# Kernel tuning notes

Measured on AMD Instinct MI355X. Metric: run time of the kernel, lower is better.

Reference implementation:

```python
import jax, jax.numpy as jnp
import numpy as np

B, N, H, HID, LOCALITY = 2, 4096, 4, 256, 30.0
VD = HID // H
F32_MAX = jnp.finfo(jnp.float32).max


def setup_inputs() -> dict:
    key = jax.random.key(0)
    k1, k2, k3, k4 = jax.random.split(key, 4)
    m_dist = jax.random.uniform(k1, (B, N, N), dtype=jnp.float32)  # pairwise distances (b,N,N)
    x = jax.random.normal(k2, (B, N, HID), dtype=jnp.float32)
    r = jax.random.normal(k3, (1, H, 1, 1), dtype=jnp.float32)  # learned per-head distance scale
    # lecun_normal: std = 1/sqrt(fan_in), fan_in = HID
    weight = jax.random.normal(k4, (H, HID, VD), dtype=jnp.float32) / np.sqrt(HID)
    return {"m_dist": m_dist, "x": x, "r": r, "weight": weight}


def reference(m_dist, x, r, weight):
    # scaled distance per head: (b,h,n,n)
    scaled = m_dist[:, None, :, :] * (r ** 2)
    # percentile-thresholded local mask (linear interpolation, per row)
    thresh = jnp.percentile(scaled, LOCALITY, axis=-1, keepdims=True, method="linear")
    scaled = jnp.where(scaled <= thresh, scaled, F32_MAX)
    att = jax.nn.softmax(-scaled, axis=-1)  # (b,h,n,n)
    value = jnp.einsum("bnj,hjk->bhnk", x, weight)  # (b,h,n,v)
    out = jnp.einsum("bhnj,bhjd->bhnd", att, value)  # (b,h,n,v)
    out = jnp.transpose(out, (0, 2, 1, 3)).reshape(out.shape[0], -1, HID)  # (b,n,hid)
    return jax.nn.gelu(out, approximate=False)
```

## Files before the change

kernel.cpp:

```cpp
#include <hip/hip_runtime.h>
#include <hip/hip_bf16.h>

#define Bc   2
#define Nc   4096
#define Hc   4
#define HIDc 256
#define VDc  64

typedef short s8v  __attribute__((ext_vector_type(8)));
typedef float f4v  __attribute__((ext_vector_type(4)));

#define XSP 260

__global__ __launch_bounds__(256) void value_kernel(
    const float* __restrict__ x, const float* __restrict__ wgt,
    unsigned short* __restrict__ vt_g)
{
    __shared__ float xs[64 * XSP];
    __shared__ unsigned short ob[64 * 64];

    int t  = threadIdx.x;
    int bid = blockIdx.x;
    int nt = bid & 63;
    int h  = (bid >> 6) & 3;
    int b  = bid >> 8;
    int n0 = nt * 64;

    const float* xg = x + ((size_t)b * Nc + n0) * HIDc;
    #pragma unroll
    for (int i = 0; i < 16; i++) {
        int id = t + i * 256;
        int row = id >> 6, ch = id & 63;
        *(float4*)&xs[row * XSP + ch * 4] = ((const float4*)xg)[id];
    }
    __syncthreads();

    int k4 = t & 15;
    int ns = t >> 4;
    const float4* wg4 = (const float4*)(wgt + (size_t)h * HIDc * VDc);

    float4 acc[4];
    #pragma unroll
    for (int i = 0; i < 4; i++) acc[i] = (float4){0.f, 0.f, 0.f, 0.f};

    for (int j = 0; j < HIDc; j += 4) {
        float4 w0 = wg4[(j + 0) * 16 + k4];
        float4 w1 = wg4[(j + 1) * 16 + k4];
        float4 w2 = wg4[(j + 2) * 16 + k4];
        float4 w3 = wg4[(j + 3) * 16 + k4];
        #pragma unroll
        for (int i = 0; i < 4; i++) {
            float4 xv = *(const float4*)&xs[(ns + i * 16) * XSP + j];
            acc[i].x += xv.x * w0.x + xv.y * w1.x + xv.z * w2.x + xv.w * w3.x;
            acc[i].y += xv.x * w0.y + xv.y * w1.y + xv.z * w2.y + xv.w * w3.y;
            acc[i].z += xv.x * w0.z + xv.y * w1.z + xv.z * w2.z + xv.w * w3.z;
            acc[i].w += xv.x * w0.w + xv.y * w1.w + xv.z * w2.w + xv.w * w3.w;
        }
    }
    #pragma unroll
    for (int i = 0; i < 4; i++) {
        int nn = ns + i * 16;
        float a[4] = {acc[i].x, acc[i].y, acc[i].z, acc[i].w};
        #pragma unroll
        for (int c = 0; c < 4; c++) {
            __hip_bfloat16 hb = __float2bfloat16(a[c]);
            ob[(k4 * 4 + c) * 64 + nn] = *(unsigned short*)&hb;
        }
    }
    __syncthreads();

    unsigned short* vg = vt_g + (((size_t)b * Hc + h) * VDc) * Nc + n0;
    #pragma unroll
    for (int i = 0; i < 16; i++) {
        int idx = t + i * 256;
        int kk = idx >> 6, nn = idx & 63;
        vg[(size_t)kk * Nc + nn] = ob[idx];
    }
}

__global__ __launch_bounds__(256) void thresh_kernel(
    const float* __restrict__ m_dist,
    float* __restrict__ thr_out, float* __restrict__ min_out)
{
    __shared__ unsigned int hist[1024];
    __shared__ float wredf[4];
    __shared__ unsigned int wsum[4];
    __shared__ unsigned int wscan[4];
    __shared__ int b0s, b1s;
    __shared__ unsigned int c0s;
    __shared__ unsigned int ncand;
    __shared__ float cand[256];
    __shared__ float s0s, s1s;

    int t = threadIdx.x;
    size_t rowid = blockIdx.x;
    const float* row = m_dist + rowid * Nc;

    float4 vals[4];
    float lmin = 1e30f;
    #pragma unroll
    for (int i = 0; i < 4; i++) {
        float4 v = ((const float4*)row)[t + i * 256];
        vals[i] = v;
        lmin = fminf(lmin, fminf(fminf(v.x, v.y), fminf(v.z, v.w)));
    }
    #pragma unroll
    for (int o = 32; o > 0; o >>= 1) lmin = fminf(lmin, __shfl_xor(lmin, o));
    if ((t & 63) == 0) wredf[t >> 6] = lmin;

    const unsigned int R0 = 1228u, R1 = 1229u;
    float wlo = 0.25f, whi = 0.35f;
    int b0 = 0, b1 = 0;
    unsigned int C0 = 0;

    for (;;) {
        float wscale = 1024.0f / (whi - wlo);

        for (int i = t; i < 1024; i += 256) hist[i] = 0u;
        if (t == 0) ncand = 0u;
        __syncthreads();

        unsigned int cb = 0;
        #pragma unroll
        for (int i = 0; i < 4; i++) {
            float a[4] = {vals[i].x, vals[i].y, vals[i].z, vals[i].w};
            #pragma unroll
            for (int j = 0; j < 4; j++) {
                float v = a[j];
                if (v < wlo) {
                    cb++;
                } else {
                    int bx = (int)((v - wlo) * wscale);
                    if (bx < 1024) atomicAdd(&hist[bx], 1u);
                }
            }
        }
        #pragma unroll
        for (int o = 32; o > 0; o >>= 1) cb += __shfl_xor(cb, o);
        if ((t & 63) == 0) wsum[t >> 6] = cb;
        __syncthreads();
        unsigned int Cb = wsum[0] + wsum[1] + wsum[2] + wsum[3];

        unsigned int c[4], csum = 0;
        #pragma unroll
        for (int j = 0; j < 4; j++) { c[j] = hist[t * 4 + j]; csum += c[j]; }
        unsigned int inc = csum;
        #pragma unroll
        for (int o = 1; o < 64; o <<= 1) {
            unsigned int nv = __shfl_up(inc, o);
            if ((t & 63) >= o) inc += nv;
        }
        if ((t & 63) == 63) wscan[t >> 6] = inc;
        __syncthreads();
        unsigned int wpref = 0;
        for (int wv = 0; wv < (t >> 6); wv++) wpref += wscan[wv];
        unsigned int T = wscan[0] + wscan[1] + wscan[2] + wscan[3];
        unsigned int P = Cb + wpref + inc - csum;

        unsigned int cum = P;
        #pragma unroll
        for (int j = 0; j < 4; j++) {
            unsigned int lo = cum, hi = cum + c[j];
            if (R0 >= lo && R0 < hi) { b0s = t * 4 + j; c0s = lo; }
            if (R1 >= lo && R1 < hi) { b1s = t * 4 + j; }
            cum = hi;
        }
        __syncthreads();

        if (Cb <= R0 && R1 < Cb + T) { b0 = b0s; b1 = b1s; C0 = c0s; break; }
        wlo = 0.0f; whi = 1.001f;
    }

    float wscale = 1024.0f / (whi - wlo);
    #pragma unroll
    for (int i = 0; i < 4; i++) {
        float a[4] = {vals[i].x, vals[i].y, vals[i].z, vals[i].w};
        #pragma unroll
        for (int j = 0; j < 4; j++) {
            float v = a[j];
            if (v >= wlo) {
                int bx = (int)((v - wlo) * wscale);
                if (bx >= b0 && bx <= b1) {
                    unsigned int p = atomicAdd(&ncand, 1u);
                    if (p < 256u) cand[p] = v;
                }
            }
        }
    }
    __syncthreads();
    unsigned int nc = min(ncand, 256u);
    if ((unsigned int)t < nc) {
        float v = cand[t];
        unsigned int rk = C0;
        for (unsigned int j = 0; j < nc; j++) {
            float u = cand[j];
            rk += (u < v || (u == v && j < (unsigned int)t)) ? 1u : 0u;
        }
        if (rk == R0) s0s = v;
        if (rk == R1) s1s = v;
    }
    __syncthreads();
    if (t == 0) {
        thr_out[rowid] = 0.5f * (s0s + s1s);
        min_out[rowid] = fminf(fminf(wredf[0], wredf[1]), fminf(wredf[2], wredf[3]));
    }
}

#define NT 32
#define JT 64
#define BIGF 3.0e38f

__global__ __launch_bounds__(512, 8) void attn_kernel(
    const float* __restrict__ m_dist, const float* __restrict__ rr,
    const unsigned short* __restrict__ vt_g,
    const float* __restrict__ thr_g, const float* __restrict__ min_g,
    float* __restrict__ Op, float* __restrict__ Zp, int jlen)
{
    __shared__ float ms[NT * 64];
    __shared__ unsigned short vt[Hc * VDc * 64];

    int t = threadIdx.x;
    const int nblk = Bc * (Nc / NT);
    int js = blockIdx.x / nblk;
    int rb = blockIdx.x - js * nblk;
    int b  = rb >> 7;
    int n0 = (rb & 127) * NT;
    int j0 = js * jlen;

    int lane = t & 63, q = lane >> 4, m16 = lane & 15;
    int w = t >> 6;
    int h = w & 3, rh = w >> 2;
    int row = rh * 16 + m16;

    float mn = min_g[b * Nc + n0 + row];
    float rv = rr[h];
    float cc = -(rv * rv) * 1.4426950408889634f;
    float nmncc = -mn * cc;

    f4v acc[4];
    #pragma unroll
    for (int ct = 0; ct < 4; ct++) acc[ct] = (f4v){0.f, 0.f, 0.f, 0.f};
    float zacc = 0.f;

    const float* mbase = m_dist + ((size_t)b * Nc + n0) * Nc + j0;
    const unsigned short* vtb = vt_g + ((size_t)b * Hc * VDc) * Nc + j0;

    int mrow = t >> 4, mch = t & 15;
    int msw  = mrow * 64 + ((mch ^ (mrow & 15)) << 2);
    float thm = thr_g[b * Nc + n0 + mrow];

    int srowl   = lane >> 3;
    int schunk8 = ((lane & 7) ^ srowl) * 8;
    unsigned short* vt_wbase = &vt[(w * 8) * 64];

    int a00 = row * 64 + (((q * 2 + 0) ^ m16) << 2);
    int a01 = row * 64 + (((q * 2 + 1) ^ m16) << 2);
    int a10 = row * 64 + (((8 + q * 2 + 0) ^ m16) << 2);
    int a11 = row * 64 + (((8 + q * 2 + 1) ^ m16) << 2);

    for (int jt = 0; jt < jlen; jt += JT) {
        #pragma unroll
        for (int i = 0; i < 4; i++) {
            int rrow = w * 8 + srowl + i * 64;
            __builtin_amdgcn_global_load_lds(
                (const __attribute__((address_space(1))) void*)
                    (vtb + (size_t)rrow * Nc + jt + schunk8),
                (__attribute__((address_space(3))) void*)
                    (vt_wbase + i * 64 * 64),
                16, 0, 0);
        }
        {
            float4 v = *(const float4*)(mbase + (size_t)mrow * Nc + jt + mch * 4);
            v.x = (v.x <= thm) ? v.x : BIGF;
            v.y = (v.y <= thm) ? v.y : BIGF;
            v.z = (v.z <= thm) ? v.z : BIGF;
            v.w = (v.w <= thm) ? v.w : BIGF;
            *(float4*)&ms[msw] = v;
        }
        __syncthreads();

        const unsigned short* vb = &vt[(h * VDc) * 64];
        #pragma unroll
        for (int ks = 0; ks < 2; ks++) {
            float4 a0 = *(const float4*)&ms[ks ? a10 : a00];
            float4 a1 = *(const float4*)&ms[ks ? a11 : a01];
            float w0 = __builtin_amdgcn_exp2f(__builtin_fmaf(a0.x, cc, nmncc));
            float w1 = __builtin_amdgcn_exp2f(__builtin_fmaf(a0.y, cc, nmncc));
            float w2 = __builtin_amdgcn_exp2f(__builtin_fmaf(a0.z, cc, nmncc));
            float w3 = __builtin_amdgcn_exp2f(__builtin_fmaf(a0.w, cc, nmncc));
            float w4 = __builtin_amdgcn_exp2f(__builtin_fmaf(a1.x, cc, nmncc));
            float w5 = __builtin_amdgcn_exp2f(__builtin_fmaf(a1.y, cc, nmncc));
            float w6 = __builtin_amdgcn_exp2f(__builtin_fmaf(a1.z, cc, nmncc));
            float w7 = __builtin_amdgcn_exp2f(__builtin_fmaf(a1.w, cc, nmncc));
            zacc += ((w0 + w1) + (w2 + w3)) + ((w4 + w5) + (w6 + w7));
            union { s8v v; __hip_bfloat162 h2[4]; } afu;
            afu.h2[0] = __float22bfloat162_rn((float2){w0, w1});
            afu.h2[1] = __float22bfloat162_rn((float2){w2, w3});
            afu.h2[2] = __float22bfloat162_rn((float2){w4, w5});
            afu.h2[3] = __float22bfloat162_rn((float2){w6, w7});
            #pragma unroll
            for (int ct = 0; ct < 4; ct++) {
                int brow = ct * 16 + m16;
                s8v bf = *(const s8v*)(vb + brow * 64 + (((ks * 4 + q) ^ (m16 & 7)) << 3));
                acc[ct] = __builtin_amdgcn_mfma_f32_16x16x32_bf16(afu.v, bf, acc[ct], 0, 0, 0);
            }
        }
        __syncthreads();
    }

    zacc += __shfl_xor(zacc, 16);
    zacc += __shfl_xor(zacc, 32);
    if (q == 0)
        Zp[(((size_t)js * Bc + b) * Hc + h) * Nc + n0 + row] = zacc;

    #pragma unroll
    for (int ct = 0; ct < 4; ct++) {
        #pragma unroll
        for (int rg = 0; rg < 4; rg++) {
            int nl = rh * 16 + q * 4 + rg;
            Op[(((size_t)js * Bc + b) * Nc + n0 + nl) * HIDc + h * VDc + ct * 16 + m16]
                = acc[ct][rg];
        }
    }
}

__global__ __launch_bounds__(256) void combine_kernel(
    const float* __restrict__ Op, const float* __restrict__ Zp,
    float* __restrict__ out, int S)
{
    int g = blockIdx.x * 256 + threadIdx.x;
    int c4 = g & 63;
    int n  = (g >> 6) & (Nc - 1);
    int b  = g >> 18;
    int h  = c4 >> 4;

    float z = 0.f;
    float4 v = {0.f, 0.f, 0.f, 0.f};
    for (int s = 0; s < S; s++) {
        z += Zp[(((size_t)s * Bc + b) * Hc + h) * Nc + n];
        float4 p = *(const float4*)&Op[(((size_t)s * Bc + b) * Nc + n) * HIDc + c4 * 4];
        v.x += p.x; v.y += p.y; v.z += p.z; v.w += p.w;
    }
    float iz = 1.0f / z;
    float4 o;
    float u;
    u = v.x * iz; o.x = 0.5f * u * (1.0f + erff(u * 0.7071067811865476f));
    u = v.y * iz; o.y = 0.5f * u * (1.0f + erff(u * 0.7071067811865476f));
    u = v.z * iz; o.z = 0.5f * u * (1.0f + erff(u * 0.7071067811865476f));
    u = v.w * iz; o.w = 0.5f * u * (1.0f + erff(u * 0.7071067811865476f));
    *(float4*)&out[(((size_t)b * Nc + n) * HIDc) + c4 * 4] = o;
}

extern "C" void kernel_launch(void* const* d_in, const int* in_sizes, int n_in,
                              void* d_out, int out_size, void* d_ws, size_t ws_size,
                              hipStream_t stream) {
    const float* m_dist = (const float*)d_in[0];
    const float* x      = (const float*)d_in[1];
    const float* r      = (const float*)d_in[2];
    const float* weight = (const float*)d_in[3];
    float* out = (float*)d_out;

    char* ws = (char*)d_ws;
    const size_t MB = 1024 * 1024;
    unsigned short* vt = (unsigned short*)ws;
    float* thr = (float*)(ws + 4 * MB);
    float* mn  = (float*)(ws + 4 * MB + 32 * 1024);
    float* Zp  = (float*)(ws + 4 * MB + 64 * 1024);
    float* Op  = (float*)(ws + 5 * MB);

    int S = 4;
    if (ws_size < 5 * MB + 4 * (size_t)(Bc * Nc * HIDc * 4)) S = 2;
    if (ws_size < 5 * MB + 2 * (size_t)(Bc * Nc * HIDc * 4)) S = 1;
    int jlen = Nc / S;

    value_kernel<<<512, 256, 0, stream>>>(x, weight, vt);
    thresh_kernel<<<Bc * Nc, 256, 0, stream>>>(m_dist, thr, mn);
    attn_kernel<<<S * Bc * (Nc / NT), 512, 0, stream>>>(m_dist, r, vt, thr, mn, Op, Zp, jlen);
    combine_kernel<<<(Bc * Nc * HIDc) / 1024, 256, 0, stream>>>(Op, Zp, out, S);
}
```

Measured before the change: 275.5 us.

## Use split-bf16 MFMA for value projection and double attention row tile

The FP32 scalar value projection becomes a prep kernel that splits x and the weights into high and low bf16 parts. A value kernel then computes the product with three bf16 MFMAs per tile (hi*hi, lo*hi, hi*lo), keeping near-FP32 accuracy on matrix cores. Separately, the attention kernel processes 64 query rows per 1024-thread block instead of 32 rows per 512 threads, so each staged V tile in LDS is reused by twice as many rows. This costs an extra kernel launch, more workspace, and possibly lower occupancy from the larger blocks.

```diff
diff --git a/kernel.cpp b/kernel.cpp
--- a/kernel.cpp
+++ b/kernel.cpp
@@ -10,15 +10,58 @@
 typedef short s8v  __attribute__((ext_vector_type(8)));
 typedef float f4v  __attribute__((ext_vector_type(4)));
 
-#define XSP 260
+static __device__ __forceinline__ unsigned short bf16bits(float f) {
+    __hip_bfloat16 h = __float2bfloat16(f);
+    return *(unsigned short*)&h;
+}
+
+__global__ __launch_bounds__(256) void prep_kernel(
+    const float* __restrict__ x, const float* __restrict__ wgt,
+    unsigned short* __restrict__ xh, unsigned short* __restrict__ xl,
+    unsigned short* __restrict__ wh, unsigned short* __restrict__ wl)
+{
+    int t = threadIdx.x, bid = blockIdx.x;
+    if (bid < 1024) {
+        size_t g = ((size_t)bid * 256 + t) * 8;
+        float4 v0 = *(const float4*)(x + g);
+        float4 v1 = *(const float4*)(x + g + 4);
+        float f[8] = {v0.x, v0.y, v0.z, v0.w, v1.x, v1.y, v1.z, v1.w};
+        union { s8v v; unsigned short u[8]; } hs, ls;
+        #pragma unroll
+        for (int i = 0; i < 8; i++) {
+            __hip_bfloat16 hb = __float2bfloat16(f[i]);
+            float hf = __bfloat162float(hb);
+            hs.u[i] = *(unsigned short*)&hb;
+            ls.u[i] = bf16bits(f[i] - hf);
+        }
+        *(s8v*)(xh + g) = hs.v;
+        *(s8v*)(xl + g) = ls.v;
+    } else {
+        int b2 = bid - 1024;
+        int h  = b2 >> 5;
+        int kt = (b2 >> 3) & 3;
+        int jc = b2 & 7;
+        int lane = t >> 2, ii = t & 3;
+        #pragma unroll
+        for (int u = 0; u < 2; u++) {
+            int i = ii * 2 + u;
+            int j = jc * 32 + (lane >> 4) * 8 + i;
+            int k = kt * 16 + (lane & 15);
+            float v = wgt[((size_t)h * HIDc + j) * VDc + k];
+            __hip_bfloat16 hb = __float2bfloat16(v);
+            float hf = __bfloat162float(hb);
+            size_t o = ((((size_t)h * 4 + kt) * 8 + jc) * 64 + lane) * 8 + i;
+            wh[o] = *(unsigned short*)&hb;
+            wl[o] = bf16bits(v - hf);
+        }
+    }
+}
 
 __global__ __launch_bounds__(256) void value_kernel(
-    const float* __restrict__ x, const float* __restrict__ wgt,
+    const unsigned short* __restrict__ xh, const unsigned short* __restrict__ xl,
+    const unsigned short* __restrict__ wh, const unsigned short* __restrict__ wl,
     unsigned short* __restrict__ vt_g)
 {
-    __shared__ float xs[64 * XSP];
-    __shared__ unsigned short ob[64 * 64];
-
     int t  = threadIdx.x;
     int bid = blockIdx.x;
     int nt = bid & 63;
@@ -26,55 +69,39 @@
     int b  = bid >> 8;
     int n0 = nt * 64;
 
-    const float* xg = x + ((size_t)b * Nc + n0) * HIDc;
-    #pragma unroll
-    for (int i = 0; i < 16; i++) {
-        int id = t + i * 256;
-        int row = id >> 6, ch = id & 63;
-        *(float4*)&xs[row * XSP + ch * 4] = ((const float4*)xg)[id];
-    }
-    __syncthreads();
-
-    int k4 = t & 15;
-    int ns = t >> 4;
-    const float4* wg4 = (const float4*)(wgt + (size_t)h * HIDc * VDc);
-
-    float4 acc[4];
-    #pragma unroll
-    for (int i = 0; i < 4; i++) acc[i] = (float4){0.f, 0.f, 0.f, 0.f};
-
-    for (int j = 0; j < HIDc; j += 4) {
-        float4 w0 = wg4[(j + 0) * 16 + k4];
-        float4 w1 = wg4[(j + 1) * 16 + k4];
-        float4 w2 = wg4[(j + 2) * 16 + k4];
-        float4 w3 = wg4[(j + 3) * 16 + k4];
-        #pragma unroll
-        for (int i = 0; i < 4; i++) {
-            float4 xv = *(const float4*)&xs[(ns + i * 16) * XSP + j];
-            acc[i].x += xv.x * w0.x + xv.y * w1.x + xv.z * w2.x + xv.w * w3.x;
-            acc[i].y += xv.x * w0.y + xv.y * w1.y + xv.z * w2.y + xv.w * w3.y;
-            acc[i].z += xv.x * w0.z + xv.y * w1.z + xv.z * w2.z + xv.w * w3.z;
-            acc[i].w += xv.x * w0.w + xv.y * w1.w + xv.z * w2.w + xv.w * w3.w;
-        }
-    }
-    #pragma unroll
-    for (int i = 0; i < 4; i++) {
-        int nn = ns + i * 16;
-        float a[4] = {acc[i].x, acc[i].y, acc[i].z, acc[i].w};
-        #pragma unroll
-        for (int c = 0; c < 4; c++) {
-            __hip_bfloat16 hb = __float2bfloat16(a[c]);
-            ob[(k4 * 4 + c) * 64 + nn] = *(unsigned short*)&hb;
-        }
-    }
-    __syncthreads();
-
-    unsigned short* vg = vt_g + (((size_t)b * Hc + h) * VDc) * Nc + n0;
-    #pragma unroll
-    for (int i = 0; i < 16; i++) {
-        int idx = t + i * 256;
-        int kk = idx >> 6, nn = idx & 63;
-        vg[(size_t)kk * Nc + nn] = ob[idx];
+    int w = t >> 6, lane = t & 63, q4 = lane >> 4, m16 = lane & 15;
+    int nb = n0 + w * 16;
+
+    const unsigned short* xhp = xh + ((size_t)(b * Nc + nb + m16)) * HIDc + q4 * 8;
+    const unsigned short* xlp = xl + ((size_t)(b * Nc + nb + m16)) * HIDc + q4 * 8;
+
+    f4v acc[4];
+    #pragma unroll
+    for (int kt = 0; kt < 4; kt++) acc[kt] = (f4v){0.f, 0.f, 0.f, 0.f};
+
+    #pragma unroll
+    for (int jc = 0; jc < 8; jc++) {
+        s8v bh = *(const s8v*)(xhp + jc * 32);
+        s8v bl = *(const s8v*)(xlp + jc * 32);
+        #pragma unroll
+        for (int kt = 0; kt < 4; kt++) {
+            size_t ao = (((size_t)(h * 4 + kt) * 8 + jc) << 9) + lane * 8;
+            s8v ah = *(const s8v*)(wh + ao);
+            s8v al = *(const s8v*)(wl + ao);
+            acc[kt] = __builtin_amdgcn_mfma_f32_16x16x32_bf16(ah, bh, acc[kt], 0, 0, 0);
+            acc[kt] = __builtin_amdgcn_mfma_f32_16x16x32_bf16(al, bh, acc[kt], 0, 0, 0);
+            acc[kt] = __builtin_amdgcn_mfma_f32_16x16x32_bf16(ah, bl, acc[kt], 0, 0, 0);
+        }
+    }
+
+    unsigned short* vg = vt_g + (((size_t)b * Hc + h) * VDc) * Nc;
+    #pragma unroll
+    for (int kt = 0; kt < 4; kt++) {
+        #pragma unroll
+        for (int rg = 0; rg < 4; rg++) {
+            int k = kt * 16 + q4 * 4 + rg;
+            vg[(size_t)k * Nc + nb + m16] = bf16bits(acc[kt][rg]);
+        }
     }
 }
 
@@ -206,11 +233,11 @@
     }
 }
 
-#define NT 32
+#define NT 64
 #define JT 64
 #define BIGF 3.0e38f
 
-__global__ __launch_bounds__(512, 8) void attn_kernel(
+__global__ __launch_bounds__(1024, 8) void attn_kernel(
     const float* __restrict__ m_dist, const float* __restrict__ rr,
     const unsigned short* __restrict__ vt_g,
     const float* __restrict__ thr_g, const float* __restrict__ min_g,
@@ -223,14 +250,14 @@
     const int nblk = Bc * (Nc / NT);
     int js = blockIdx.x / nblk;
     int rb = blockIdx.x - js * nblk;
-    int b  = rb >> 7;
-    int n0 = (rb & 127) * NT;
+    int b  = rb >> 6;
+    int n0 = (rb & 63) * NT;
     int j0 = js * jlen;
 
     int lane = t & 63, q = lane >> 4, m16 = lane & 15;
     int w = t >> 6;
-    int h = w & 3, rh = w >> 2;
-    int row = rh * 16 + m16;
+    int h = w & 3, rq = w >> 2;
+    int row = rq * 16 + m16;
 
     float mn = min_g[b * Nc + n0 + row];
     float rv = rr[h];
@@ -249,8 +276,7 @@
     int msw  = mrow * 64 + ((mch ^ (mrow & 15)) << 2);
     float thm = thr_g[b * Nc + n0 + mrow];
 
-    int srowl   = lane >> 3;
-    int schunk8 = ((lane & 7) ^ srowl) * 8;
+    int schunk8 = ((t & 7) ^ ((t >> 3) & 7)) * 8;
     unsigned short* vt_wbase = &vt[(w * 8) * 64];
 
     int a00 = row * 64 + (((q * 2 + 0) ^ m16) << 2);
@@ -260,13 +286,13 @@
 
     for (int jt = 0; jt < jlen; jt += JT) {
         #pragma unroll
-        for (int i = 0; i < 4; i++) {
-            int rrow = w * 8 + srowl + i * 64;
+        for (int i = 0; i < 2; i++) {
+            int rrow = (t >> 3) + i * 128;
             __builtin_amdgcn_global_load_lds(
                 (const __attribute__((address_space(1))) void*)
                     (vtb + (size_t)rrow * Nc + jt + schunk8),
                 (__attribute__((address_space(3))) void*)
-                    (vt_wbase + i * 64 * 64),
+                    (vt_wbase + i * 128 * 64),
                 16, 0, 0);
         }
         {
@@ -317,7 +343,7 @@
     for (int ct = 0; ct < 4; ct++) {
         #pragma unroll
         for (int rg = 0; rg < 4; rg++) {
-            int nl = rh * 16 + q * 4 + rg;
+            int nl = rq * 16 + q * 4 + rg;
             Op[(((size_t)js * Bc + b) * Nc + n0 + nl) * HIDc + h * VDc + ct * 16 + m16]
                 = acc[ct][rg];
         }
@@ -369,12 +395,19 @@
     float* Op  = (float*)(ws + 5 * MB);
 
     int S = 4;
-    if (ws_size < 5 * MB + 4 * (size_t)(Bc * Nc * HIDc * 4)) S = 2;
-    if (ws_size < 5 * MB + 2 * (size_t)(Bc * Nc * HIDc * 4)) S = 1;
+    if (ws_size < 14 * MB + 4 * (size_t)(Bc * Nc * HIDc * 4)) S = 2;
+    if (ws_size < 14 * MB + 2 * (size_t)(Bc * Nc * HIDc * 4)) S = 1;
     int jlen = Nc / S;
 
-    value_kernel<<<512, 256, 0, stream>>>(x, weight, vt);
+    char* pb = ws + 5 * MB + (size_t)S * (Bc * Nc * HIDc * 4);
+    unsigned short* xh = (unsigned short*)pb;
+    unsigned short* xl = (unsigned short*)(pb + 4 * MB);
+    unsigned short* wh = (unsigned short*)(pb + 8 * MB);
+    unsigned short* wl = (unsigned short*)(pb + 8 * MB + 128 * 1024);
+
+    prep_kernel<<<1152, 256, 0, stream>>>(x, weight, xh, xl, wh, wl);
+    value_kernel<<<512, 256, 0, stream>>>(xh, xl, wh, wl, vt);
     thresh_kernel<<<Bc * Nc, 256, 0, stream>>>(m_dist, thr, mn);
-    attn_kernel<<<S * Bc * (Nc / NT), 512, 0, stream>>>(m_dist, r, vt, thr, mn, Op, Zp, jlen);
+    attn_kernel<<<S * Bc * (Nc / NT), 1024, 0, stream>>>(m_dist, r, vt, thr, mn, Op, Zp, jlen);
     combine_kernel<<<(Bc * Nc * HIDc) / 1024, 256, 0, stream>>>(Op, Zp, out, S);
 }
```

After: 266.8 us. 3.2% less time.
